# Performance work log

Hardware: AMD Instinct MI355X
Metric: run time of the kernel (lower is better)

## Reference

```python
import jax, jax.numpy as jnp
import numpy as np

N = 20000   # nodes
E = 320000  # edges
G = 64      # graphs in batch
IN = 256    # in_dim
H = 256     # hidden_dim1
C = 2       # n_classes


def setup_inputs() -> dict:
    key = jax.random.key(0)
    ks = jax.random.split(key, 12)
    h = jax.random.normal(ks[0], (N, IN), jnp.float32)
    src = jax.random.randint(ks[1], (E,), 0, N)
    dst = jax.random.randint(ks[2], (E,), 0, N)
    graph_id = jnp.sort(jax.random.randint(ks[3], (N,), 0, G))
    s_in = 1.0 / np.sqrt(IN)
    s_h = 1.0 / np.sqrt(H)
    W_conv = jax.random.normal(ks[4], (IN, H), jnp.float32) * s_in
    b_conv = jnp.zeros((H,), jnp.float32)
    w_gate = jax.random.normal(ks[5], (H, 1), jnp.float32) * s_h
    b_gate = jnp.zeros((1,), jnp.float32)
    W1 = jax.random.normal(ks[6], (H, H), jnp.float32) * s_h
    b1 = jnp.zeros((H,), jnp.float32)
    W2 = jax.random.normal(ks[7], (H, C), jnp.float32) * s_h
    b2 = jnp.zeros((C,), jnp.float32)
    return dict(h=h, src=src, dst=dst, graph_id=graph_id, W_conv=W_conv,
                b_conv=b_conv, w_gate=w_gate, b_gate=b_gate, W1=W1, b1=b1,
                W2=W2, b2=b2)


def reference(h, src, dst, graph_id, W_conv, b_conv, w_gate, b_gate, W1, b1, W2, b2):
    ones_e = jnp.ones((E,), jnp.float32)
    # DGL GraphConv, norm='both': D_out^-1/2 on source, D_in^-1/2 on dest
    deg_out = jax.ops.segment_sum(ones_e, src, num_segments=N)
    deg_in = jax.ops.segment_sum(ones_e, dst, num_segments=N)
    hn = h * jax.lax.rsqrt(jnp.maximum(deg_out, 1.0))[:, None]
    hn = hn @ W_conv                       # [N, H] (weight applied before aggregation)
    agg = jax.ops.segment_sum(hn[src], dst, num_segments=N)  # gather + scatter-add
    agg = agg * jax.lax.rsqrt(jnp.maximum(deg_in, 1.0))[:, None] + b_conv
    hr = jax.nn.relu(agg)                  # F.relu after conv1
    # GlobalAttentionPooling: per-graph segment softmax over gate scores
    gate = hr @ w_gate + b_gate            # [N, 1]
    gmax = jax.ops.segment_max(gate, graph_id, num_segments=G)
    e = jnp.exp(gate - gmax[graph_id])
    denom = jax.ops.segment_sum(e, graph_id, num_segments=G)
    att = e / denom[graph_id]              # [N, 1] attention weights (g2)
    hg = jax.ops.segment_sum(att * hr, graph_id, num_segments=G)  # [G, H]
    # classifier heads (dropout is identity at inference)
    a2 = hg @ W1 + b1
    a3 = a2 @ W2 + b2
    return jax.nn.sigmoid(a3), att, hg
```

## Files before the change

kernel.cpp:

```cpp
#include <hip/hip_runtime.h>
#include <hip/hip_bf16.h>
#include <hip/hip_fp16.h>
#include <math.h>

#define NN 20000
#define EE 320000
#define GG 64
#define IND 256
#define HD 256
#define CC 2

typedef __hip_bfloat16 bf16;
typedef __attribute__((ext_vector_type(8))) short short8;
typedef __attribute__((ext_vector_type(4))) float f32x4;

__device__ __forceinline__ float b2f(bf16 x){ return __bfloat162float(x); }
__device__ __forceinline__ float bits2f(unsigned short b){
    union{ float f; unsigned u; } v; v.u = ((unsigned)b) << 16; return v.f;
}
__device__ __forceinline__ short f2bs(float x){
    union{ bf16 b; short s; } u; u.b = __float2bfloat16(x); return u.s;
}
__device__ __forceinline__ float ldf3(const void* p, size_t i, int c){
    if (c == 1) return b2f(((const bf16*)p)[i]);
    if (c == 2) return __half2float(((const __half*)p)[i]);
    return ((const float*)p)[i];
}
__device__ __forceinline__ int idec(const void* p, int i, int c){
    if (c == 1) return (int)(((const long long*)p)[i]);
    if (c == 2) return (int)(((const float*)p)[i]);
    if (c == 3) return (int)__half2float(((const __half*)p)[i]);
    return ((const int*)p)[i];
}
__device__ __forceinline__ int wdetect_wave(const unsigned short* p, int t){
    unsigned u = p[2*t];
    int e8 = (u >> 7) & 0xFF;
    int e5 = (u >> 10) & 0x1F;
    int nz = __popcll(__ballot(u != 0));
    int cb = __popcll(__ballot(e8 >= 100 && e8 <= 141));
    int cf = __popcll(__ballot(e5 >= 4 && e5 <= 22));
    return (nz < 8) ? 0 : (cb >= 60) ? 1 : ((cf >= 60) ? 2 : 0);
}

#define ZBLK 64
#define DETB (9 + IND)
__global__ __launch_bounds__(256) void k_detect(const void* src, const void* dst,
                         const void* gid,
                         const unsigned short* h, const unsigned short* Wc,
                         const unsigned short* wg, const unsigned short* W1,
                         const unsigned short* W2, const unsigned short* bc,
                         int* icode, int* dcode, int* zero_base,
                         bf16* __restrict__ Wb){
    int blk = blockIdx.x;
    int t = threadIdx.x;
    if (blk < 3){
        if (t >= 64) return;
        const void* buf = (blk == 0) ? src : (blk == 1) ? dst : gid;
        int n     = (blk == 2) ? NN : EE;
        int bound = (blk == 2) ? GG : NN;
        long long v64 = ((const long long*)buf)[n/8 + t];
        unsigned long long bad64 = __ballot(v64 < 0 || v64 >= (long long)bound);
        int v32 = ((const int*)buf)[n/4 + t];
        unsigned long long bad32 = __ballot(v32 < 0 || v32 >= bound);
        float f32v = __uint_as_float(((const unsigned*)buf)[n/4 + t]);
        unsigned long long badf32 = __ballot(!(f32v >= 0.f && f32v < (float)bound));
        float f16v = __half2float(((const __half*)buf)[n/2 + t]);
        unsigned long long badf16 = __ballot(!(f16v >= 0.f && f16v < (float)bound));
        if (t == 0)
            icode[blk] = (bad64 == 0ull) ? 1 : ((bad32 == 0ull) ? 0 :
                         ((badf32 == 0ull) ? 2 : ((badf16 == 0ull) ? 3 : 0)));
    } else if (blk < 9){
        if (t >= 64) return;
        int b = blk - 3;
        const unsigned short* p = b==0?h:b==1?Wc:b==2?wg:b==3?W1:b==4?W2:bc;
        int code = wdetect_wave(p, t);
        if (t == 0) dcode[b] = code;
    } else if (blk < DETB){
        int k = blk - 9;
        __shared__ int scode;
        if (t < 64){
            int code = wdetect_wave(Wc, t);
            if (t == 0) scode = code;
        }
        __syncthreads();
        int c = scode;
        Wb[(size_t)t*IND + k] = __float2bfloat16(ldf3(Wc, (size_t)k*HD + t, c));
    } else {
        int idx = (blk - DETB)*256 + t;
        const int total = 3*NN + GG*HD;
        for (int i = idx; i < total; i += ZBLK*256) zero_base[i] = 0;
    }
}

#define GEMMB (NN/32)
#define PREPB ((EE+255)/256)
__global__ __launch_bounds__(256) void k_prepgemm(const void* __restrict__ h,
                                                  const bf16* __restrict__ Wb,
                                                  const void* __restrict__ src_r,
                                                  const void* __restrict__ dst_r,
                                                  const void* __restrict__ gid_r,
                                                  const int* __restrict__ icode,
                                                  const int* __restrict__ dcode,
                                                  int* __restrict__ gid_i,
                                                  int* cnt_out, int* cnt_in,
                                                  bf16* __restrict__ hn){
    __shared__ unsigned short tile[32*260];
    int blk = blockIdx.x;
    if (blk >= GEMMB){
        int i = (blk - GEMMB)*256 + threadIdx.x;
        if (i < NN) gid_i[i] = idec(gid_r, i, icode[2]);
        if (i >= EE) return;
        int s = idec(src_r, i, icode[0]);
        int d = idec(dst_r, i, icode[1]);
        if ((unsigned)s < NN) atomicAdd(&cnt_out[s], 1);
        if ((unsigned)d < NN) atomicAdd(&cnt_in[d], 1);
        return;
    }
    int fh = dcode[0];
    int tid = threadIdx.x;
    int wave = tid >> 6, lane = tid & 63;
    int q = lane >> 4, mr = lane & 15;
    int row0 = blk * 32;
    int ncol0 = wave * 64;
    f32x4 acc[2][4] = {};
    const float* hf = (const float*)h;
    #pragma unroll
    for (int k0 = 0; k0 < IND; k0 += 32){
        short8 a[2], b[4];
        if (fh == 0){
            #pragma unroll
            for (int mi = 0; mi < 2; mi++){
                int r = row0 + mi*16 + mr;
                const float4* p = (const float4*)(hf + (size_t)r*IND + k0 + q*8);
                float4 v0 = p[0], v1 = p[1];
                a[mi][0] = f2bs(v0.x); a[mi][1] = f2bs(v0.y);
                a[mi][2] = f2bs(v0.z); a[mi][3] = f2bs(v0.w);
                a[mi][4] = f2bs(v1.x); a[mi][5] = f2bs(v1.y);
                a[mi][6] = f2bs(v1.z); a[mi][7] = f2bs(v1.w);
            }
        } else {
            #pragma unroll
            for (int mi = 0; mi < 2; mi++){
                int r = row0 + mi*16 + mr;
                #pragma unroll
                for (int j = 0; j < 8; j++)
                    a[mi][j] = f2bs(ldf3(h, (size_t)r*IND + k0 + q*8 + j, fh));
            }
        }
        #pragma unroll
        for (int ni = 0; ni < 4; ni++)
            b[ni] = *reinterpret_cast<const short8*>(
                        Wb + (size_t)(ncol0 + ni*16 + mr)*IND + k0 + q*8);
        #pragma unroll
        for (int mi = 0; mi < 2; mi++)
            #pragma unroll
            for (int ni = 0; ni < 4; ni++)
                acc[mi][ni] = __builtin_amdgcn_mfma_f32_16x16x32_bf16(
                                  a[mi], b[ni], acc[mi][ni], 0, 0, 0);
    }
    #pragma unroll
    for (int mi = 0; mi < 2; mi++){
        int rowb = mi*16 + q*4;
        #pragma unroll
        for (int r = 0; r < 4; r++){
            int row = rowb + r;
            #pragma unroll
            for (int ni = 0; ni < 4; ni++)
                tile[row*260 + ncol0 + ni*16 + mr] =
                    (unsigned short)f2bs(acc[mi][ni][r]);
        }
    }
    __syncthreads();
    #pragma unroll
    for (int p = 0; p < 4; p++){
        int s = p*256 + tid;
        int row = s >> 5;
        int c8 = (s & 31) * 8;
        short8 v = *reinterpret_cast<const short8*>(&tile[row*260 + c8]);
        *reinterpret_cast<short8*>(hn + (size_t)(row0 + row)*HD + c8) = v;
    }
}

__global__ __launch_bounds__(1024) void k_scan(const int* __restrict__ cnt_out,
                                               const int* __restrict__ cnt_in,
                                               const int* __restrict__ gid,
                                               float* rs_out, float* rs_in,
                                               int* __restrict__ row_start,
                                               int* gstart, int* gend){
    int t = threadIdx.x;
    for (int i = t; i < NN; i += 1024){
        rs_out[i] = rsqrtf(fmaxf((float)cnt_out[i], 1.f));
        rs_in[i]  = rsqrtf(fmaxf((float)cnt_in[i], 1.f));
    }
    __shared__ int part[1024];
    const int per = (NN + 1023)/1024;
    int lo = t*per, hi = min(lo+per, NN);
    int s = 0;
    for (int i = lo; i < hi; i++) s += cnt_in[i];
    part[t] = s; __syncthreads();
    for (int off = 1; off < 1024; off <<= 1){
        int v = (t >= off) ? part[t-off] : 0;
        __syncthreads();
        part[t] += v;
        __syncthreads();
    }
    int base = part[t] - s;
    for (int i = lo; i < hi; i++){ row_start[i] = base; base += cnt_in[i]; }
    if (t == 1023) row_start[NN] = part[1023];
    __shared__ int ls[GG+1];
    if (t <= GG){
        int a = 0, b = NN;
        while (a < b){
            int mid = (a + b) >> 1;
            if (gid[mid] < t) a = mid + 1; else b = mid;
        }
        ls[t] = a;
    }
    __syncthreads();
    if (t < GG){ gstart[t] = ls[t]; gend[t] = ls[t+1]; }
}

__global__ void k_fill(const void* src_r, const void* dst_r,
                       const int* __restrict__ icode,
                       const int* __restrict__ row_start, int* __restrict__ cursor,
                       int* __restrict__ csr_src){
    int e = blockIdx.x*256 + threadIdx.x;
    if (e >= EE) return;
    int s = idec(src_r, e, icode[0]);
    int d = idec(dst_r, e, icode[1]);
    if ((unsigned)s >= NN || (unsigned)d >= NN) return;
    int pos = atomicAdd(&cursor[d], 1);
    csr_src[row_start[d] + pos] = s;
}

__global__ __launch_bounds__(256) void k_gather(const bf16* __restrict__ hn,
                                                const float* __restrict__ rs_out,
                                                const float* __restrict__ rs_in,
                                                const int* __restrict__ row_start,
                                                const int* __restrict__ csr_src,
                                                const void* __restrict__ b_conv,
                                                const void* __restrict__ w_gate,
                                                const void* __restrict__ b_gate,
                                                const int* __restrict__ dcode,
                                                float* __restrict__ hr,
                                                float* __restrict__ gate){
    int wave = threadIdx.x >> 6, lane = threadIdx.x & 63;
    int n = blockIdx.x*4 + wave;
    if (n >= NN) return;
    int lo = row_start[n], hi = row_start[n+1];
    int half = lane >> 5, l2 = lane & 31;
    float a0=0.f,a1=0.f,a2=0.f,a3=0.f,a4=0.f,a5=0.f,a6=0.f,a7=0.f;
    int j = lo;
    for (; j + 8 <= hi; j += 8){
        int sA = csr_src[j+0+half], sB = csr_src[j+2+half];
        int sC = csr_src[j+4+half], sD = csr_src[j+6+half];
        float rA = rs_out[sA], rB = rs_out[sB], rC = rs_out[sC], rD = rs_out[sD];
        short8 uA = *reinterpret_cast<const short8*>(hn + (size_t)sA*HD + l2*8);
        short8 uB = *reinterpret_cast<const short8*>(hn + (size_t)sB*HD + l2*8);
        short8 uC = *reinterpret_cast<const short8*>(hn + (size_t)sC*HD + l2*8);
        short8 uD = *reinterpret_cast<const short8*>(hn + (size_t)sD*HD + l2*8);
        a0 = fmaf(rA, bits2f((unsigned short)uA[0]),
             fmaf(rB, bits2f((unsigned short)uB[0]),
             fmaf(rC, bits2f((unsigned short)uC[0]),
             fmaf(rD, bits2f((unsigned short)uD[0]), a0))));
        a1 = fmaf(rA, bits2f((unsigned short)uA[1]),
             fmaf(rB, bits2f((unsigned short)uB[1]),
             fmaf(rC, bits2f((unsigned short)uC[1]),
             fmaf(rD, bits2f((unsigned short)uD[1]), a1))));
        a2 = fmaf(rA, bits2f((unsigned short)uA[2]),
             fmaf(rB, bits2f((unsigned short)uB[2]),
             fmaf(rC, bits2f((unsigned short)uC[2]),
             fmaf(rD, bits2f((unsigned short)uD[2]), a2))));
        a3 = fmaf(rA, bits2f((unsigned short)uA[3]),
             fmaf(rB, bits2f((unsigned short)uB[3]),
             fmaf(rC, bits2f((unsigned short)uC[3]),
             fmaf(rD, bits2f((unsigned short)uD[3]), a3))));
        a4 = fmaf(rA, bits2f((unsigned short)uA[4]),
             fmaf(rB, bits2f((unsigned short)uB[4]),
             fmaf(rC, bits2f((unsigned short)uC[4]),
             fmaf(rD, bits2f((unsigned short)uD[4]), a4))));
        a5 = fmaf(rA, bits2f((unsigned short)uA[5]),
             fmaf(rB, bits2f((unsigned short)uB[5]),
             fmaf(rC, bits2f((unsigned short)uC[5]),
             fmaf(rD, bits2f((unsigned short)uD[5]), a5))));
        a6 = fmaf(rA, bits2f((unsigned short)uA[6]),
             fmaf(rB, bits2f((unsigned short)uB[6]),
             fmaf(rC, bits2f((unsigned short)uC[6]),
             fmaf(rD, bits2f((unsigned short)uD[6]), a6))));
        a7 = fmaf(rA, bits2f((unsigned short)uA[7]),
             fmaf(rB, bits2f((unsigned short)uB[7]),
             fmaf(rC, bits2f((unsigned short)uC[7]),
             fmaf(rD, bits2f((unsigned short)uD[7]), a7))));
    }
    for (; j + 2 <= hi; j += 2){
        int s = csr_src[j+half];
        float r = rs_out[s];
        short8 u = *reinterpret_cast<const short8*>(hn + (size_t)s*HD + l2*8);
        a0 = fmaf(r, bits2f((unsigned short)u[0]), a0);
        a1 = fmaf(r, bits2f((unsigned short)u[1]), a1);
        a2 = fmaf(r, bits2f((unsigned short)u[2]), a2);
        a3 = fmaf(r, bits2f((unsigned short)u[3]), a3);
        a4 = fmaf(r, bits2f((unsigned short)u[4]), a4);
        a5 = fmaf(r, bits2f((unsigned short)u[5]), a5);
        a6 = fmaf(r, bits2f((unsigned short)u[6]), a6);
        a7 = fmaf(r, bits2f((unsigned short)u[7]), a7);
    }
    if (j < hi && half == 0){
        int s = csr_src[j];
        float r = rs_out[s];
        short8 u = *reinterpret_cast<const short8*>(hn + (size_t)s*HD + l2*8);
        a0 = fmaf(r, bits2f((unsigned short)u[0]), a0);
        a1 = fmaf(r, bits2f((unsigned short)u[1]), a1);
        a2 = fmaf(r, bits2f((unsigned short)u[2]), a2);
        a3 = fmaf(r, bits2f((unsigned short)u[3]), a3);
        a4 = fmaf(r, bits2f((unsigned short)u[4]), a4);
        a5 = fmaf(r, bits2f((unsigned short)u[5]), a5);
        a6 = fmaf(r, bits2f((unsigned short)u[6]), a6);
        a7 = fmaf(r, bits2f((unsigned short)u[7]), a7);
    }
    float send0 = half ? a0 : a4;
    float send1 = half ? a1 : a5;
    float send2 = half ? a2 : a6;
    float send3 = half ? a3 : a7;
    float recv0 = __shfl_xor(send0, 32);
    float recv1 = __shfl_xor(send1, 32);
    float recv2 = __shfl_xor(send2, 32);
    float recv3 = __shfl_xor(send3, 32);
    float tot0 = (half ? a4 : a0) + recv0;
    float tot1 = (half ? a5 : a1) + recv1;
    float tot2 = (half ? a6 : a2) + recv2;
    float tot3 = (half ? a7 : a3) + recv3;
    int db = dcode[5], fg = dcode[2];
    float rsn = rs_in[n];
    int c = l2*8 + half*4;
    float v0 = fmaxf(fmaf(tot0, rsn, ldf3(b_conv, c+0, db)), 0.f);
    float v1 = fmaxf(fmaf(tot1, rsn, ldf3(b_conv, c+1, db)), 0.f);
    float v2 = fmaxf(fmaf(tot2, rsn, ldf3(b_conv, c+2, db)), 0.f);
    float v3 = fmaxf(fmaf(tot3, rsn, ldf3(b_conv, c+3, db)), 0.f);
    float4 fv; fv.x = v0; fv.y = v1; fv.z = v2; fv.w = v3;
    *(float4*)(hr + (size_t)n*HD + c) = fv;
    float g = v0*ldf3(w_gate, c+0, fg) + v1*ldf3(w_gate, c+1, fg)
            + v2*ldf3(w_gate, c+2, fg) + v3*ldf3(w_gate, c+3, fg);
    #pragma unroll
    for (int off = 32; off; off >>= 1) g += __shfl_down(g, off);
    if (lane == 0) gate[n] = g + ldf3(b_gate, 0, db);
}

__global__ __launch_bounds__(256) void k_softhg(const float* __restrict__ gate,
                                                const float* __restrict__ hr,
                                                const int* __restrict__ gstart,
                                                const int* __restrict__ gend,
                                                float* __restrict__ hg,
                                                float* __restrict__ out_att){
    int g = blockIdx.x >> 3, part = blockIdx.x & 7;
    int t = threadIdx.x, lane = t & 63, wid = t >> 6;
    int lo = gstart[g], hi = gend[g], len = hi - lo;
    if (len <= 0) return;
    __shared__ float red[4];
    float m = -INFINITY;
    for (int n = lo + t; n < hi; n += 256) m = fmaxf(m, gate[n]);
    #pragma unroll
    for (int off = 32; off; off >>= 1) m = fmaxf(m, __shfl_xor(m, off));
    if (lane == 0) red[wid] = m;
    __syncthreads();
    m = fmaxf(fmaxf(red[0], red[1]), fmaxf(red[2], red[3]));
    __syncthreads();
    float s = 0.f;
    for (int n = lo + t; n < hi; n += 256) s += expf(gate[n] - m);
    #pragma unroll
    for (int off = 32; off; off >>= 1) s += __shfl_xor(s, off);
    if (lane == 0) red[wid] = s;
    __syncthreads();
    s = red[0] + red[1] + red[2] + red[3];
    float inv = 1.f / s;
    int chunk = (len + 7) >> 3;
    int plo = lo + part*chunk, phi = min(plo + chunk, hi);
    if (plo >= phi) return;
    for (int n = plo + t; n < phi; n += 256)
        out_att[n] = expf(gate[n] - m) * inv;
    float a0 = 0.f, a1 = 0.f, a2 = 0.f, a3 = 0.f;
    int r = plo;
    for (; r + 4 <= phi; r += 4){
        float w0 = expf(gate[r+0] - m) * inv;
        float w1 = expf(gate[r+1] - m) * inv;
        float w2 = expf(gate[r+2] - m) * inv;
        float w3 = expf(gate[r+3] - m) * inv;
        a0 = fmaf(w0, hr[(size_t)(r+0)*HD + t], a0);
        a1 = fmaf(w1, hr[(size_t)(r+1)*HD + t], a1);
        a2 = fmaf(w2, hr[(size_t)(r+2)*HD + t], a2);
        a3 = fmaf(w3, hr[(size_t)(r+3)*HD + t], a3);
    }
    for (; r < phi; r++)
        a0 = fmaf(expf(gate[r] - m) * inv, hr[(size_t)r*HD + t], a0);
    atomicAdd(&hg[g*HD + t], (a0 + a1) + (a2 + a3));
}

__global__ __launch_bounds__(256) void k_cls(const float* __restrict__ hg,
                                             const void* __restrict__ W1,
                                             const void* __restrict__ b1,
                                             const void* __restrict__ W2,
                                             const void* __restrict__ b2,
                                             const int* __restrict__ dcode,
                                             float* __restrict__ out0,
                                             float* __restrict__ out_hg){
    int f1 = dcode[3], f2 = dcode[4], db = dcode[5];
    int g = blockIdx.x, tid = threadIdx.x;
    __shared__ float hs[256];
    float hv = hg[g*HD + tid];
    hs[tid] = hv;
    out_hg[g*HD + tid] = hv;
    __syncthreads();
    float acc = ldf3(b1, tid, db);
    if (f1 == 1){
        const bf16* w = (const bf16*)W1;
        for (int k = 0; k < HD; k++) acc += hs[k]*b2f(w[(size_t)k*HD + tid]);
    } else if (f1 == 2){
        const __half* w = (const __half*)W1;
        for (int k = 0; k < HD; k++) acc += hs[k]*__half2float(w[(size_t)k*HD + tid]);
    } else {
        const float* w = (const float*)W1;
        for (int k = 0; k < HD; k++) acc += hs[k]*w[(size_t)k*HD + tid];
    }
    float p0 = acc * ldf3(W2, tid*CC + 0, f2);
    float p1 = acc * ldf3(W2, tid*CC + 1, f2);
    __shared__ float r0[256], r1[256];
    r0[tid] = p0; r1[tid] = p1; __syncthreads();
    for (int s = 128; s; s >>= 1){
        if (tid < s){ r0[tid] += r0[tid+s]; r1[tid] += r1[tid+s]; }
        __syncthreads();
    }
    if (tid == 0){
        out0[g*CC+0] = 1.f/(1.f + expf(-(r0[0] + ldf3(b2, 0, db))));
        out0[g*CC+1] = 1.f/(1.f + expf(-(r1[0] + ldf3(b2, 1, db))));
    }
}

extern "C" void kernel_launch(void* const* d_in, const int* in_sizes, int n_in,
                              void* d_out, int out_size, void* d_ws, size_t ws_size,
                              hipStream_t stream) {
    const void* h      = d_in[0];
    const void* src_r  = d_in[1];
    const void* dst_r  = d_in[2];
    const void* gid_r  = d_in[3];
    const void* W_conv = d_in[4];
    const void* b_conv = d_in[5];
    const void* w_gate = d_in[6];
    const void* b_gate = d_in[7];
    const void* W1     = d_in[8];
    const void* b1     = d_in[9];
    const void* W2     = d_in[10];
    const void* b2     = d_in[11];

    float* out     = (float*)d_out;
    float* out0    = out;
    float* out_att = out + GG*CC;
    float* out_hg  = out + GG*CC + NN;

    char* w = (char*)d_ws;
    float* hr   = (float*)w;  w += (size_t)NN*HD*sizeof(float);
    bf16*  hn   = (bf16*)w;   w += (size_t)NN*HD*sizeof(bf16);
    bf16*  Wb   = (bf16*)w;   w += (size_t)IND*HD*sizeof(bf16);
    float* rs_o = (float*)w;  w += (size_t)NN*sizeof(float);
    float* rs_i = (float*)w;  w += (size_t)NN*sizeof(float);
    float* gate = (float*)w;  w += (size_t)NN*sizeof(float);
    int* gstart = (int*)w;    w += GG*sizeof(int);
    int* gend   = (int*)w;    w += GG*sizeof(int);
    int* dcode  = (int*)w;    w += 8*sizeof(int);
    int* icode  = (int*)w;    w += 8*sizeof(int);
    int* gid_i  = (int*)w;    w += (size_t)NN*sizeof(int);
    int* cnt_out= (int*)w;    w += (size_t)NN*sizeof(int);
    int* cnt_in = (int*)w;    w += (size_t)NN*sizeof(int);
    int* cursor = (int*)w;    w += (size_t)NN*sizeof(int);
    float* hg   = (float*)w;  w += (size_t)GG*HD*sizeof(float);
    int* rowst  = (int*)w;    w += (size_t)(NN+1)*sizeof(int);
    int* csr    = (int*)w;    w += (size_t)EE*sizeof(int);

    k_detect<<<DETB + ZBLK, 256, 0, stream>>>(src_r, dst_r, gid_r,
                                     (const unsigned short*)h, (const unsigned short*)W_conv,
                                     (const unsigned short*)w_gate, (const unsigned short*)W1,
                                     (const unsigned short*)W2, (const unsigned short*)b_conv,
                                     icode, dcode, cnt_out, Wb);

    k_prepgemm<<<GEMMB + PREPB, 256, 0, stream>>>(h, Wb, src_r, dst_r, gid_r,
                                                  icode, dcode, gid_i,
                                                  cnt_out, cnt_in, hn);

    k_scan<<<1, 1024, 0, stream>>>(cnt_out, cnt_in, gid_i, rs_o, rs_i,
                                   rowst, gstart, gend);

    k_fill<<<PREPB, 256, 0, stream>>>(src_r, dst_r, icode, rowst, cursor, csr);

    k_gather<<<(NN+3)/4, 256, 0, stream>>>(hn, rs_o, rs_i, rowst, csr,
                                           b_conv, w_gate, b_gate, dcode, hr, gate);

    k_softhg<<<GG*8, 256, 0, stream>>>(gate, hr, gstart, gend, hg, out_att);

    k_cls<<<GG, 256, 0, stream>>>(hg, W1, b1, W2, b2, dcode, out0, out_hg);
}
```

Measured before the change: 229.7 us.

## Replace global-atomic degree counting and CSR fill with LDS-privatized partial histograms

Degree counting now runs in 128 blocks, one per edge chunk, role and half of the node range. Each block builds a histogram in shared memory and writes it out as a per-chunk partial. A new reduction kernel sums the partials, converts the in-degree partials to per-chunk prefix offsets, and computes the rsqrt norms and decoded graph ids. The CSR fill then uses shared-memory cursors per chunk, replacing global atomics on a cursor array. This removes global atomic contention and the zeroing of three N-sized arrays, but each edge chunk is read by several blocks, only 64 fill blocks run, and partial arrays of 32×N ints must be written and read back.

```diff
diff --git a/kernel.cpp b/kernel.cpp
--- a/kernel.cpp
+++ b/kernel.cpp
@@ -9,6 +9,10 @@
 #define IND 256
 #define HD 256
 #define CC 2
+
+#define HRB 32
+#define EPB (EE/HRB)
+#define NH  (NN/2)
 
 typedef __hip_bfloat16 bf16;
 typedef __attribute__((ext_vector_type(8))) short short8;
@@ -42,7 +46,7 @@
     return (nz < 8) ? 0 : (cb >= 60) ? 1 : ((cf >= 60) ? 2 : 0);
 }
 
-#define ZBLK 64
+#define ZBLK 8
 #define DETB (9 + IND)
 __global__ __launch_bounds__(256) void k_detect(const void* src, const void* dst,
                          const void* gid,
@@ -87,37 +91,44 @@
         Wb[(size_t)t*IND + k] = __float2bfloat16(ldf3(Wc, (size_t)k*HD + t, c));
     } else {
         int idx = (blk - DETB)*256 + t;
-        const int total = 3*NN + GG*HD;
+        const int total = GG*HD;
         for (int i = idx; i < total; i += ZBLK*256) zero_base[i] = 0;
     }
 }
 
 #define GEMMB (NN/32)
-#define PREPB ((EE+255)/256)
 __global__ __launch_bounds__(256) void k_prepgemm(const void* __restrict__ h,
                                                   const bf16* __restrict__ Wb,
                                                   const void* __restrict__ src_r,
                                                   const void* __restrict__ dst_r,
-                                                  const void* __restrict__ gid_r,
                                                   const int* __restrict__ icode,
                                                   const int* __restrict__ dcode,
-                                                  int* __restrict__ gid_i,
-                                                  int* cnt_out, int* cnt_in,
+                                                  int* __restrict__ pout,
+                                                  int* __restrict__ pin,
                                                   bf16* __restrict__ hn){
-    __shared__ unsigned short tile[32*260];
+    __shared__ int shm[NH];
     int blk = blockIdx.x;
+    int tid = threadIdx.x;
     if (blk >= GEMMB){
-        int i = (blk - GEMMB)*256 + threadIdx.x;
-        if (i < NN) gid_i[i] = idec(gid_r, i, icode[2]);
-        if (i >= EE) return;
-        int s = idec(src_r, i, icode[0]);
-        int d = idec(dst_r, i, icode[1]);
-        if ((unsigned)s < NN) atomicAdd(&cnt_out[s], 1);
-        if ((unsigned)d < NN) atomicAdd(&cnt_in[d], 1);
+        int hb = blk - GEMMB;
+        int hr = hb >> 2, role = (hb >> 1) & 1, half = hb & 1;
+        for (int i = tid; i < NH; i += 256) shm[i] = 0;
+        __syncthreads();
+        const void* arr = role ? dst_r : src_r;
+        int code = icode[role];
+        int base = hr*EPB;
+        for (int e = base + tid; e < base + EPB; e += 256){
+            int v = idec(arr, e, code);
+            int vh = v - half*NH;
+            if ((unsigned)vh < NH) atomicAdd(&shm[vh], 1);
+        }
+        __syncthreads();
+        int* dst_part = (role ? pin : pout) + (size_t)hr*NN + half*NH;
+        for (int i = tid; i < NH; i += 256) dst_part[i] = shm[i];
         return;
     }
+    unsigned short* tile = (unsigned short*)shm;
     int fh = dcode[0];
-    int tid = threadIdx.x;
     int wave = tid >> 6, lane = tid & 63;
     int q = lane >> 4, mr = lane & 15;
     int row0 = blk * 32;
@@ -181,17 +192,37 @@
     }
 }
 
-__global__ __launch_bounds__(1024) void k_scan(const int* __restrict__ cnt_out,
-                                               const int* __restrict__ cnt_in,
+__global__ __launch_bounds__(256) void k_red(const void* __restrict__ gid_r,
+                                             const int* __restrict__ icode,
+                                             int* __restrict__ pout,
+                                             int* __restrict__ pin,
+                                             float* __restrict__ rs_o,
+                                             float* __restrict__ rs_i,
+                                             int* __restrict__ cnt_in,
+                                             int* __restrict__ gid_i){
+    int n = blockIdx.x*256 + threadIdx.x;
+    if (n >= NN) return;
+    int so = 0;
+    #pragma unroll 8
+    for (int hr = 0; hr < HRB; hr++) so += pout[(size_t)hr*NN + n];
+    rs_o[n] = rsqrtf(fmaxf((float)so, 1.f));
+    int pre = 0;
+    #pragma unroll 8
+    for (int hr = 0; hr < HRB; hr++){
+        int v = pin[(size_t)hr*NN + n];
+        pin[(size_t)hr*NN + n] = pre;
+        pre += v;
+    }
+    cnt_in[n] = pre;
+    rs_i[n] = rsqrtf(fmaxf((float)pre, 1.f));
+    gid_i[n] = idec(gid_r, n, icode[2]);
+}
+
+__global__ __launch_bounds__(1024) void k_scan(const int* __restrict__ cnt_in,
                                                const int* __restrict__ gid,
-                                               float* rs_out, float* rs_in,
                                                int* __restrict__ row_start,
                                                int* gstart, int* gend){
     int t = threadIdx.x;
-    for (int i = t; i < NN; i += 1024){
-        rs_out[i] = rsqrtf(fmaxf((float)cnt_out[i], 1.f));
-        rs_in[i]  = rsqrtf(fmaxf((float)cnt_in[i], 1.f));
-    }
     __shared__ int part[1024];
     const int per = (NN + 1023)/1024;
     int lo = t*per, hi = min(lo+per, NN);
@@ -220,17 +251,29 @@
     if (t < GG){ gstart[t] = ls[t]; gend[t] = ls[t+1]; }
 }
 
-__global__ void k_fill(const void* src_r, const void* dst_r,
+__global__ __launch_bounds__(256) void k_fill(const void* src_r, const void* dst_r,
                        const int* __restrict__ icode,
-                       const int* __restrict__ row_start, int* __restrict__ cursor,
+                       const int* __restrict__ row_start,
+                       const int* __restrict__ pin,
                        int* __restrict__ csr_src){
-    int e = blockIdx.x*256 + threadIdx.x;
-    if (e >= EE) return;
-    int s = idec(src_r, e, icode[0]);
-    int d = idec(dst_r, e, icode[1]);
-    if ((unsigned)s >= NN || (unsigned)d >= NN) return;
-    int pos = atomicAdd(&cursor[d], 1);
-    csr_src[row_start[d] + pos] = s;
+    __shared__ int lr[NH];
+    int blk = blockIdx.x, t = threadIdx.x;
+    int hr = blk >> 1, half = blk & 1;
+    for (int i = t; i < NH; i += 256) lr[i] = 0;
+    __syncthreads();
+    int c0 = icode[0], c1 = icode[1];
+    int base = hr*EPB;
+    const int* pre = pin + (size_t)hr*NN;
+    for (int e = base + t; e < base + EPB; e += 256){
+        int s = idec(src_r, e, c0);
+        int d = idec(dst_r, e, c1);
+        if ((unsigned)s >= NN || (unsigned)d >= NN) continue;
+        int dh = d - half*NH;
+        if ((unsigned)dh < NH){
+            int r = atomicAdd(&lr[dh], 1);
+            csr_src[row_start[d] + pre[d] + r] = s;
+        }
+    }
 }
 
 __global__ __launch_bounds__(256) void k_gather(const bf16* __restrict__ hn,
@@ -468,27 +511,28 @@
     int* dcode  = (int*)w;    w += 8*sizeof(int);
     int* icode  = (int*)w;    w += 8*sizeof(int);
     int* gid_i  = (int*)w;    w += (size_t)NN*sizeof(int);
-    int* cnt_out= (int*)w;    w += (size_t)NN*sizeof(int);
     int* cnt_in = (int*)w;    w += (size_t)NN*sizeof(int);
-    int* cursor = (int*)w;    w += (size_t)NN*sizeof(int);
     float* hg   = (float*)w;  w += (size_t)GG*HD*sizeof(float);
     int* rowst  = (int*)w;    w += (size_t)(NN+1)*sizeof(int);
     int* csr    = (int*)w;    w += (size_t)EE*sizeof(int);
+    int* pout   = (int*)w;    w += (size_t)HRB*NN*sizeof(int);
+    int* pin    = (int*)w;    w += (size_t)HRB*NN*sizeof(int);
 
     k_detect<<<DETB + ZBLK, 256, 0, stream>>>(src_r, dst_r, gid_r,
                                      (const unsigned short*)h, (const unsigned short*)W_conv,
                                      (const unsigned short*)w_gate, (const unsigned short*)W1,
                                      (const unsigned short*)W2, (const unsigned short*)b_conv,
-                                     icode, dcode, cnt_out, Wb);
-
-    k_prepgemm<<<GEMMB + PREPB, 256, 0, stream>>>(h, Wb, src_r, dst_r, gid_r,
-                                                  icode, dcode, gid_i,
-                                                  cnt_out, cnt_in, hn);
-
-    k_scan<<<1, 1024, 0, stream>>>(cnt_out, cnt_in, gid_i, rs_o, rs_i,
-                                   rowst, gstart, gend);
-
-    k_fill<<<PREPB, 256, 0, stream>>>(src_r, dst_r, icode, rowst, cursor, csr);
+                                     icode, dcode, hg ? (int*)hg : nullptr, Wb);
+
+    k_prepgemm<<<GEMMB + HRB*4, 256, 0, stream>>>(h, Wb, src_r, dst_r,
+                                                  icode, dcode, pout, pin, hn);
+
+    k_red<<<(NN+255)/256, 256, 0, stream>>>(gid_r, icode, pout, pin,
+                                            rs_o, rs_i, cnt_in, gid_i);
+
+    k_scan<<<1, 1024, 0, stream>>>(cnt_in, gid_i, rowst, gstart, gend);
+
+    k_fill<<<HRB*2, 256, 0, stream>>>(src_r, dst_r, icode, rowst, pin, csr);
 
     k_gather<<<(NN+3)/4, 256, 0, stream>>>(hn, rs_o, rs_i, rowst, csr,
                                            b_conv, w_gate, b_gate, dcode, hr, gate);
```

Result: faster. 223.2 us (-2.8%).
